# Kernel tuning notes

Measured on AMD Instinct MI355X. Metric: run time of the kernel, lower is better.

Reference implementation:

```python
import jax, jax.numpy as jnp
import numpy as np

HEADS = 8

def setup_inputs() -> dict:
    key = jax.random.key(0)
    k1, k2, k3 = jax.random.split(key, 3)
    B, C, L = 8, 512, 4096
    dim_head = 64
    hidden = HEADS * dim_head  # 512
    x = jax.random.normal(k1, (B, C, L), dtype=jnp.float32)
    # Conv1d(dim, hidden*3, 1, bias=False) -> weight [hidden*3, dim]
    w_qkv = jax.random.normal(k2, (hidden * 3, C), dtype=jnp.float32) * 0.02
    # Conv1d(hidden, dim, 1) -> weight [dim, hidden], bias [dim]
    w_out = jax.random.normal(k3, (C, hidden), dtype=jnp.float32) * 0.02
    b_out = jnp.zeros((C,), dtype=jnp.float32)
    return {"x": x, "w_qkv": w_qkv, "w_out": w_out, "b_out": b_out}

def reference(x, w_qkv, w_out, b_out):
    B, C, L = x.shape
    # 1x1 Conv1d == channel matmul
    qkv = jnp.einsum('oc,bcl->bol', w_qkv, x)            # [B, 3*H*dh, L]
    qkv = qkv.reshape(B, 3, HEADS, -1, L)                # qkv outermost, then heads, then c
    q, k, v = qkv[:, 0], qkv[:, 1], qkv[:, 2]            # each [B, H, dh, L]
    k = jax.nn.softmax(k, axis=-1)                       # softmax over sequence
    context = jnp.einsum('bhdn,bhen->bhde', k, v)        # [B, H, dh, dh]
    out = jnp.einsum('bhde,bhdn->bhen', context, q)      # [B, H, dh, L]
    out = out.reshape(B, -1, L)                          # [B, H*dh, L]
    return jnp.einsum('oc,bcl->bol', w_out, out) + b_out[None, :, None]
```

## Files before the change

### kernel.cpp

```cpp
#include <hip/hip_runtime.h>
#include <hip/hip_bf16.h>


typedef __bf16 bf16x8 __attribute__((ext_vector_type(8)));
typedef __bf16 bf16x4 __attribute__((ext_vector_type(4)));
typedef float  f32x4  __attribute__((ext_vector_type(4)));

#define B_  8
#define L_  4096
#define C_  512

#define GLD_LDS16(g, l)                                             \
    __builtin_amdgcn_global_load_lds(                               \
        (const __attribute__((address_space(1))) void*)(g),         \
        (__attribute__((address_space(3))) void*)(l), 16, 0, 0)

#define FENCE asm volatile("" ::: "memory")
#define BAR   do { FENCE; __builtin_amdgcn_s_barrier(); FENCE; } while (0)
#define DRAIN_LGKM asm volatile("s_waitcnt lgkmcnt(0)" ::: "memory")
#define WAIT_VM(N) asm volatile("s_waitcnt vmcnt(" #N ")" ::: "memory")

__global__ __launch_bounds__(256) void prep_all(const float* __restrict__ x,
                                                __hip_bfloat16* __restrict__ xt,
                                                const float* __restrict__ wqkv_f,
                                                __hip_bfloat16* __restrict__ wkv_b,
                                                __hip_bfloat16* __restrict__ wqT) {
    __shared__ float tile[64 * 133];
    int blk = blockIdx.x;
    int t = threadIdx.x;
    if (blk < 2048) {
        int b = blk >> 8, rem = blk & 255;
        int l0 = (rem & 31) * 128, c0 = (rem >> 5) * 64;
        const float* xp = x + ((size_t)b * C_ + c0) * L_ + l0;
#pragma unroll
        for (int p = 0; p < 8; p++) {
            int i = p * 8 + (t >> 5);
            int j = (t & 31) * 4;
            float4 vv = *(const float4*)(xp + (size_t)i * L_ + j);
            *(float4*)&tile[i * 133 + j] = vv;
        }
        __syncthreads();
        unsigned short* xo = (unsigned short*)xt + ((size_t)b * L_ + l0) * C_ + c0;
        int cg8 = (t & 7) * 8;
#pragma unroll
        for (int qq = 0; qq < 4; qq++) {
            int l = qq * 32 + (t >> 3);
            bf16x8 ov;
#pragma unroll
            for (int k = 0; k < 8; k++) ov[k] = (__bf16)tile[(cg8 + k) * 133 + l];
            *(bf16x8*)(xo + (size_t)l * C_ + cg8) = ov;
        }
    } else if (blk < 4096) {
        int i = (blk - 2048) * 256 + t;
        wkv_b[i] = __float2bfloat16(wqkv_f[512 * 512 + i]);
    } else {
        int tb = blk - 4096;
        int r0 = (tb >> 4) * 32, c0 = (tb & 15) * 32;
        int tx = t & 31, ty = t >> 5;
        for (int r = 0; r < 32; r += 8)
            tile[(ty + r) * 33 + tx] = wqkv_f[(size_t)(r0 + ty + r) * 512 + c0 + tx];
        __syncthreads();
        for (int r = 0; r < 32; r += 8)
            wqT[(size_t)(c0 + ty + r) * 512 + r0 + tx] = __float2bfloat16(tile[tx * 33 + ty + r]);
    }
}

template <int MODE>
__global__ __launch_bounds__(256, 2) void gemm_p(
    const __hip_bfloat16* __restrict__ A, const __hip_bfloat16* __restrict__ Bt,
    size_t strideA, size_t strideB, int M, int N, int K,
    __hip_bfloat16* __restrict__ kb, __hip_bfloat16* __restrict__ vb,
    __hip_bfloat16* __restrict__ obf,
    float* __restrict__ outb, const float* __restrict__ bias) {
    __shared__ alignas(16) unsigned short sA[2][128 * 64];
    __shared__ alignas(16) unsigned short sB[2][128 * 64];

    int b = blockIdx.z;
    int m0 = blockIdx.y * 128, n0 = blockIdx.x * 128;
    const __hip_bfloat16* Ab = A + strideA * (size_t)b;
    const __hip_bfloat16* Bb = Bt + strideB * (size_t)b;

    int t = threadIdx.x;
    int lane = t & 63, wv = t >> 6;
    int l16 = lane & 15, q4 = lane >> 4;
    int wr = (wv >> 1) * 64, wc = (wv & 1) * 64;

    int srow = lane >> 3;
    int swz  = ((lane & 7) ^ srow) * 8;

    const __hip_bfloat16* gA[4];
    const __hip_bfloat16* gB[4];
    unsigned ldoff[4];
#pragma unroll
    for (int c = 0; c < 4; c++) {
        int r = c * 32 + wv * 8;
        gA[c] = Ab + (size_t)(m0 + r + srow) * K + swz;
        gB[c] = Bb + (size_t)(n0 + r + srow) * K + swz;
        ldoff[c] = (unsigned)r * 64;
    }

    int gsel0 = (q4 ^ (l16 & 7)) * 8;
    int gsel1 = gsel0 ^ 32;
    unsigned rA = (unsigned)(wr + l16) * 64;
    unsigned rB = (unsigned)(wc + l16) * 64;
    int NKT = K >> 6;

    f32x4 acc[4][4] = {};
    bf16x8 aF[4][2], bF[4][2];

#pragma unroll
    for (int c = 0; c < 4; c++) GLD_LDS16(gA[c], &sA[0][ldoff[c]]);
#pragma unroll
    for (int c = 0; c < 4; c++) GLD_LDS16(gB[c], &sB[0][ldoff[c]]);
    if (NKT > 1) {
#pragma unroll
        for (int c = 0; c < 4; c++) GLD_LDS16(gA[c] + 64, &sA[1][ldoff[c]]);
        WAIT_VM(4);
    } else {
        WAIT_VM(0);
    }
    BAR;

#pragma unroll 1
    for (int kt = 0; kt < NKT; ++kt) {
        int cur = kt & 1, nbuf = cur ^ 1;
        const unsigned short* As_b = sA[cur];
        const unsigned short* Bs_b = sB[cur];
        bool st1 = (kt + 1) < NKT;
        bool st2 = (kt + 2) < NKT;

#pragma unroll
        for (int i = 0; i < 4; i++) {
            aF[i][0] = *(const bf16x8*)&As_b[rA + i * 1024 + gsel0];
            aF[i][1] = *(const bf16x8*)&As_b[rA + i * 1024 + gsel1];
        }
#pragma unroll
        for (int j = 0; j < 2; j++) {
            bF[j][0] = *(const bf16x8*)&Bs_b[rB + j * 1024 + gsel0];
            bF[j][1] = *(const bf16x8*)&Bs_b[rB + j * 1024 + gsel1];
        }
        if (st1) {
            int ko = (kt + 1) << 6;
#pragma unroll
            for (int c = 0; c < 4; c++) GLD_LDS16(gB[c] + ko, &sB[nbuf][ldoff[c]]);
        }
        BAR;
        __builtin_amdgcn_s_setprio(1);
#pragma unroll
        for (int ks = 0; ks < 2; ks++)
#pragma unroll
            for (int i = 0; i < 4; i++)
#pragma unroll
                for (int j = 0; j < 2; j++)
                    acc[i][j] = __builtin_amdgcn_mfma_f32_16x16x32_bf16(aF[i][ks], bF[j][ks], acc[i][j], 0, 0, 0);
        __builtin_amdgcn_s_setprio(0);
        DRAIN_LGKM;
        BAR;

#pragma unroll
        for (int j = 2; j < 4; j++) {
            bF[j][0] = *(const bf16x8*)&Bs_b[rB + j * 1024 + gsel0];
            bF[j][1] = *(const bf16x8*)&Bs_b[rB + j * 1024 + gsel1];
        }
        if (st2) {
            int ko = (kt + 2) << 6;
#pragma unroll
            for (int c = 0; c < 4; c++) GLD_LDS16(gA[c] + ko, &sA[cur][ldoff[c]]);
        }
        BAR;
        __builtin_amdgcn_s_setprio(1);
#pragma unroll
        for (int ks = 0; ks < 2; ks++)
#pragma unroll
            for (int i = 0; i < 4; i++)
#pragma unroll
                for (int j = 0; j < 2; j++)
                    acc[i][2 + j] = __builtin_amdgcn_mfma_f32_16x16x32_bf16(aF[i][ks], bF[2 + j][ks], acc[i][2 + j], 0, 0, 0);
        __builtin_amdgcn_s_setprio(0);
        DRAIN_LGKM;
        if (st2) { WAIT_VM(4); } else { WAIT_VM(0); }
        BAR;
    }

#pragma unroll
    for (int i = 0; i < 4; i++)
#pragma unroll
        for (int j = 0; j < 4; j++)
#pragma unroll
            for (int r = 0; r < 4; r++) {
                int row = m0 + wr + i * 16 + q4 * 4 + r;
                int col = n0 + wc + j * 16 + l16;
                float val = acc[i][j][r];
                if (MODE == 1) {
                    bool isk = (m0 < 512);
                    __hip_bfloat16* dst = isk ? kb : vb;
                    if (isk) val = __expf(val);
                    dst[((size_t)b * 512 + (row & 511)) * (size_t)N + col] = __float2bfloat16(val);
                } else if (MODE == 3) {
                    obf[((size_t)b * 512 + row) * (size_t)N + col] = __float2bfloat16(val);
                } else {
                    outb[((size_t)b * M + row) * (size_t)N + col] = val + bias[row];
                }
            }
}

__global__ __launch_bounds__(256) void ctx_kernel(const __hip_bfloat16* __restrict__ ek,
                                                  const __hip_bfloat16* __restrict__ v,
                                                  float* __restrict__ ctxp,
                                                  float* __restrict__ Sp) {
    int bx = blockIdx.x;
    int kc = bx >> 1, dh = bx & 1;
    int h = blockIdx.y, b = blockIdx.z;
    int t = threadIdx.x, lane = t & 63, wv = t >> 6;
    int l16 = lane & 15, q4 = lane >> 4;
    const __hip_bfloat16* ka = ek + ((size_t)b * 512 + h * 64 + dh * 32) * L_;
    const __hip_bfloat16* va = v + ((size_t)b * 512 + h * 64) * L_;

    f32x4 acc[2][4] = {};
    float ps[2] = {0.f, 0.f};
    int nbase = kc * 512 + wv * 128;
#pragma unroll
    for (int s = 0; s < 4; s++) {
        int n = nbase + s * 32 + q4 * 8;
        bf16x8 af[2], bfr[4];
#pragma unroll
        for (int i = 0; i < 2; i++) {
            af[i] = *(const bf16x8*)(ka + (size_t)(i * 16 + l16) * L_ + n);
#pragma unroll
            for (int e = 0; e < 8; e++) ps[i] += (float)af[i][e];
        }
#pragma unroll
        for (int j = 0; j < 4; j++)
            bfr[j] = *(const bf16x8*)(va + (size_t)(j * 16 + l16) * L_ + n);
#pragma unroll
        for (int i = 0; i < 2; i++)
#pragma unroll
            for (int j = 0; j < 4; j++)
                acc[i][j] = __builtin_amdgcn_mfma_f32_16x16x32_bf16(af[i], bfr[j], acc[i][j], 0, 0, 0);
    }

    __shared__ float sred[4][32];
#pragma unroll
    for (int i = 0; i < 2; i++) {
        ps[i] += __shfl_xor(ps[i], 16, 64);
        ps[i] += __shfl_xor(ps[i], 32, 64);
    }
    if (q4 == 0) {
#pragma unroll
        for (int i = 0; i < 2; i++) sred[wv][i * 16 + l16] = ps[i];
    }

    __shared__ float cbuf[2048];
    __syncthreads();
    for (int w = 0; w < 4; w++) {
        if (wv == w) {
#pragma unroll
            for (int i = 0; i < 2; i++)
#pragma unroll
                for (int j = 0; j < 4; j++)
#pragma unroll
                    for (int r = 0; r < 4; r++) {
                        int mm = i * 16 + q4 * 4 + r, nn = j * 16 + l16;
                        float pv = acc[i][j][r];
                        if (w == 0) cbuf[mm * 64 + nn] = pv;
                        else        cbuf[mm * 64 + nn] += pv;
                    }
        }
        __syncthreads();
    }
    float* cg = ctxp + ((size_t)kc * 64 + b * 8 + h) * 4096 + dh * 2048;
    for (int i = t; i < 2048; i += 256) cg[i] = cbuf[i];
    if (t < 32)
        Sp[((size_t)kc * 64 + b * 8 + h) * 64 + dh * 32 + t] =
            sred[0][t] + sred[1][t] + sred[2][t] + sred[3][t];
}

__global__ __launch_bounds__(256) void w2_kernel(const float* __restrict__ wout,
                                                 const float* __restrict__ ctxp,
                                                 const float* __restrict__ Sp,
                                                 __hip_bfloat16* __restrict__ w2) {
    int ob = blockIdx.x, h = blockIdx.y, b = blockIdx.z;
    __shared__ float cT[64 * 65];
    __shared__ float wT[64 * 65];
    __shared__ float Sinv[64];
    int t = threadIdx.x;
    const size_t SL = (size_t)64 * 4096;
    const float* cg = ctxp + ((size_t)b * 8 + h) * 4096;
    if (t < 64) {
        const float* sg = Sp + ((size_t)b * 8 + h) * 64;
        float S = 0.f;
#pragma unroll
        for (int s = 0; s < 8; s++) S += sg[(size_t)s * 64 * 64 + t];
        Sinv[t] = 1.0f / S;
    }
    __syncthreads();
#pragma unroll
    for (int it = 0; it < 4; ++it) {
        int i0 = (t + it * 256) * 4;
        int d = i0 >> 6, e0 = i0 & 63;
        float4 s4 = {0.f, 0.f, 0.f, 0.f};
#pragma unroll
        for (int sl = 0; sl < 8; sl++) {
            float4 vv = *(const float4*)&cg[(size_t)sl * SL + i0];
            s4.x += vv.x; s4.y += vv.y; s4.z += vv.z; s4.w += vv.w;
        }
        float si = Sinv[d];
        float4 wv4 = *(const float4*)&wout[(size_t)(ob * 64 + d) * 512 + h * 64 + e0];
        cT[(e0 + 0) * 65 + d] = s4.x * si;
        cT[(e0 + 1) * 65 + d] = s4.y * si;
        cT[(e0 + 2) * 65 + d] = s4.z * si;
        cT[(e0 + 3) * 65 + d] = s4.w * si;
        wT[(e0 + 0) * 65 + d] = wv4.x;
        wT[(e0 + 1) * 65 + d] = wv4.y;
        wT[(e0 + 2) * 65 + d] = wv4.z;
        wT[(e0 + 3) * 65 + d] = wv4.w;
    }
    __syncthreads();
    int ol = t >> 2;
    int db = (t & 3) * 16;
    unsigned short* w2p = (unsigned short*)w2 + ((size_t)b * 512 + ob * 64 + ol) * 512 + h * 64;
    for (int g = 0; g < 4; g++) {
        int d0 = db + g * 4;
        float s0 = 0.f, s1 = 0.f, s2 = 0.f, s3 = 0.f;
#pragma unroll
        for (int e = 0; e < 64; e++) {
            float w = wT[e * 65 + ol];
            s0 += w * cT[e * 65 + d0];
            s1 += w * cT[e * 65 + d0 + 1];
            s2 += w * cT[e * 65 + d0 + 2];
            s3 += w * cT[e * 65 + d0 + 3];
        }
        bf16x4 ov;
        ov[0] = (__bf16)s0; ov[1] = (__bf16)s1; ov[2] = (__bf16)s2; ov[3] = (__bf16)s3;
        *(bf16x4*)(w2p + d0) = ov;
    }
}

extern "C" void kernel_launch(void* const* d_in, const int* in_sizes, int n_in,
                              void* d_out, int out_size, void* d_ws, size_t ws_size,
                              hipStream_t stream) {
    const float* x     = (const float*)d_in[0];
    const float* w_qkv = (const float*)d_in[1];
    const float* w_out = (const float*)d_in[2];
    const float* b_out = (const float*)d_in[3];
    float* out = (float*)d_out;
    char* ws = (char*)d_ws;

    const size_t QKV = (size_t)B_ * 512 * L_;
    size_t off_xt   = 0;
    size_t off_wkv  = off_xt + (size_t)B_ * L_ * C_ * 2;
    size_t off_wqT  = off_wkv + (size_t)1024 * 512 * 2;
    size_t off_k    = off_wqT + (size_t)512 * 512 * 2;
    size_t off_v    = off_k + QKV * 2;
    size_t off_ctxp = off_v + QKV * 2;
    size_t off_Sp   = off_ctxp + (size_t)8 * 64 * 4096 * 4;
    size_t off_w2   = off_k;
    size_t off_w3   = off_k + (size_t)B_ * 512 * 512 * 2;

    __hip_bfloat16* xt   = (__hip_bfloat16*)(ws + off_xt);
    __hip_bfloat16* wkvb = (__hip_bfloat16*)(ws + off_wkv);
    __hip_bfloat16* wqT  = (__hip_bfloat16*)(ws + off_wqT);
    __hip_bfloat16* kb   = (__hip_bfloat16*)(ws + off_k);
    __hip_bfloat16* vb   = (__hip_bfloat16*)(ws + off_v);
    float*          ctxp = (float*)(ws + off_ctxp);
    float*          Sp   = (float*)(ws + off_Sp);
    __hip_bfloat16* w2   = (__hip_bfloat16*)(ws + off_w2);
    __hip_bfloat16* W3   = (__hip_bfloat16*)(ws + off_w3);

    prep_all<<<4352, 256, 0, stream>>>(x, xt, w_qkv, wkvb, wqT);

    gemm_p<1><<<dim3(L_ / 128, 1024 / 128, B_), 256, 0, stream>>>(
        wkvb, xt, 0, (size_t)L_ * C_, 1024, L_, 512, kb, vb, nullptr, nullptr, nullptr);

    ctx_kernel<<<dim3(16, 8, B_), 256, 0, stream>>>(kb, vb, ctxp, Sp);

    w2_kernel<<<dim3(8, 8, B_), 256, 0, stream>>>(w_out, ctxp, Sp, w2);

    gemm_p<3><<<dim3(512 / 128, 512 / 128, B_), 256, 0, stream>>>(
        w2, wqT, (size_t)512 * 512, 0, 512, 512, 512, nullptr, nullptr, W3, nullptr, nullptr);

    gemm_p<2><<<dim3(L_ / 128, 512 / 128, B_), 256, 0, stream>>>(
        W3, xt, (size_t)512 * 512, (size_t)L_ * C_, 512, L_, 512, nullptr, nullptr, nullptr, out, b_out);
}
```

Before: 243.6 us.

## Halve GEMM K-tile to 32 and raise occupancy to four blocks per CU

The GEMM K-tile shrinks from 64 to 32, halving LDS per block (32 KB instead of 64 KB), and launch bounds rise from 2 to 4 blocks per CU. The pipeline is restructured into one LDS read phase and one MFMA phase per iteration, with A and B for tile kt+2 both prefetched into the buffer just consumed. This aims to hide latency through more resident waves instead of intra-block interleaving. The cost is twice as many barrier-separated iterations with less MFMA work each, plus tighter register limits that could cause spills.

```diff
diff --git a/kernel.cpp b/kernel.cpp
--- a/kernel.cpp
+++ b/kernel.cpp
@@ -66,14 +66,14 @@
 }
 
 template <int MODE>
-__global__ __launch_bounds__(256, 2) void gemm_p(
+__global__ __launch_bounds__(256, 4) void gemm_p(
     const __hip_bfloat16* __restrict__ A, const __hip_bfloat16* __restrict__ Bt,
     size_t strideA, size_t strideB, int M, int N, int K,
     __hip_bfloat16* __restrict__ kb, __hip_bfloat16* __restrict__ vb,
     __hip_bfloat16* __restrict__ obf,
     float* __restrict__ outb, const float* __restrict__ bias) {
-    __shared__ alignas(16) unsigned short sA[2][128 * 64];
-    __shared__ alignas(16) unsigned short sB[2][128 * 64];
+    __shared__ alignas(16) unsigned short sA[2][128 * 32];
+    __shared__ alignas(16) unsigned short sB[2][128 * 32];
 
     int b = blockIdx.z;
     int m0 = blockIdx.y * 128, n0 = blockIdx.x * 128;
@@ -85,99 +85,70 @@
     int l16 = lane & 15, q4 = lane >> 4;
     int wr = (wv >> 1) * 64, wc = (wv & 1) * 64;
 
-    int srow = lane >> 3;
-    int swz  = ((lane & 7) ^ srow) * 8;
-
-    const __hip_bfloat16* gA[4];
-    const __hip_bfloat16* gB[4];
-    unsigned ldoff[4];
-#pragma unroll
-    for (int c = 0; c < 4; c++) {
-        int r = c * 32 + wv * 8;
-        gA[c] = Ab + (size_t)(m0 + r + srow) * K + swz;
-        gB[c] = Bb + (size_t)(n0 + r + srow) * K + swz;
-        ldoff[c] = (unsigned)r * 64;
-    }
-
-    int gsel0 = (q4 ^ (l16 & 7)) * 8;
-    int gsel1 = gsel0 ^ 32;
-    unsigned rA = (unsigned)(wr + l16) * 64;
-    unsigned rB = (unsigned)(wc + l16) * 64;
-    int NKT = K >> 6;
+    int srow = lane >> 2;
+    int swz  = ((lane & 3) ^ (srow & 3)) * 8;
+
+    const __hip_bfloat16* gA[2];
+    const __hip_bfloat16* gB[2];
+    unsigned ldoff[2];
+#pragma unroll
+    for (int c = 0; c < 2; c++) {
+        int lr = c * 64 + wv * 16 + srow;
+        gA[c] = Ab + (size_t)(m0 + lr) * K + swz;
+        gB[c] = Bb + (size_t)(n0 + lr) * K + swz;
+        ldoff[c] = (unsigned)(c * 64 + wv * 16) * 32;
+    }
+
+    int gsel = (q4 ^ (l16 & 3)) * 8;
+    unsigned rA = (unsigned)(wr + l16) * 32;
+    unsigned rB = (unsigned)(wc + l16) * 32;
+    const int NKT = K >> 5;
 
     f32x4 acc[4][4] = {};
-    bf16x8 aF[4][2], bF[4][2];
-
-#pragma unroll
-    for (int c = 0; c < 4; c++) GLD_LDS16(gA[c], &sA[0][ldoff[c]]);
-#pragma unroll
-    for (int c = 0; c < 4; c++) GLD_LDS16(gB[c], &sB[0][ldoff[c]]);
-    if (NKT > 1) {
-#pragma unroll
-        for (int c = 0; c < 4; c++) GLD_LDS16(gA[c] + 64, &sA[1][ldoff[c]]);
-        WAIT_VM(4);
-    } else {
-        WAIT_VM(0);
-    }
+    bf16x8 aF[4], bF[4];
+
+#pragma unroll
+    for (int c = 0; c < 2; c++) {
+        GLD_LDS16(gA[c], &sA[0][ldoff[c]]);
+        GLD_LDS16(gB[c], &sB[0][ldoff[c]]);
+    }
+#pragma unroll
+    for (int c = 0; c < 2; c++) {
+        GLD_LDS16(gA[c] + 32, &sA[1][ldoff[c]]);
+        GLD_LDS16(gB[c] + 32, &sB[1][ldoff[c]]);
+    }
+    WAIT_VM(4);
     BAR;
 
 #pragma unroll 1
     for (int kt = 0; kt < NKT; ++kt) {
-        int cur = kt & 1, nbuf = cur ^ 1;
+        int cur = kt & 1;
         const unsigned short* As_b = sA[cur];
         const unsigned short* Bs_b = sB[cur];
-        bool st1 = (kt + 1) < NKT;
         bool st2 = (kt + 2) < NKT;
 
 #pragma unroll
-        for (int i = 0; i < 4; i++) {
-            aF[i][0] = *(const bf16x8*)&As_b[rA + i * 1024 + gsel0];
-            aF[i][1] = *(const bf16x8*)&As_b[rA + i * 1024 + gsel1];
-        }
-#pragma unroll
-        for (int j = 0; j < 2; j++) {
-            bF[j][0] = *(const bf16x8*)&Bs_b[rB + j * 1024 + gsel0];
-            bF[j][1] = *(const bf16x8*)&Bs_b[rB + j * 1024 + gsel1];
-        }
-        if (st1) {
-            int ko = (kt + 1) << 6;
-#pragma unroll
-            for (int c = 0; c < 4; c++) GLD_LDS16(gB[c] + ko, &sB[nbuf][ldoff[c]]);
-        }
-        BAR;
-        __builtin_amdgcn_s_setprio(1);
-#pragma unroll
-        for (int ks = 0; ks < 2; ks++)
-#pragma unroll
-            for (int i = 0; i < 4; i++)
-#pragma unroll
-                for (int j = 0; j < 2; j++)
-                    acc[i][j] = __builtin_amdgcn_mfma_f32_16x16x32_bf16(aF[i][ks], bF[j][ks], acc[i][j], 0, 0, 0);
-        __builtin_amdgcn_s_setprio(0);
+        for (int i = 0; i < 4; i++) aF[i] = *(const bf16x8*)&As_b[rA + i * 512 + gsel];
+#pragma unroll
+        for (int j = 0; j < 4; j++) bF[j] = *(const bf16x8*)&Bs_b[rB + j * 512 + gsel];
         DRAIN_LGKM;
         BAR;
 
-#pragma unroll
-        for (int j = 2; j < 4; j++) {
-            bF[j][0] = *(const bf16x8*)&Bs_b[rB + j * 1024 + gsel0];
-            bF[j][1] = *(const bf16x8*)&Bs_b[rB + j * 1024 + gsel1];
-        }
         if (st2) {
-            int ko = (kt + 2) << 6;
-#pragma unroll
-            for (int c = 0; c < 4; c++) GLD_LDS16(gA[c] + ko, &sA[cur][ldoff[c]]);
-        }
-        BAR;
+            int ko = (kt + 2) << 5;
+#pragma unroll
+            for (int c = 0; c < 2; c++) {
+                GLD_LDS16(gA[c] + ko, &sA[cur][ldoff[c]]);
+                GLD_LDS16(gB[c] + ko, &sB[cur][ldoff[c]]);
+            }
+        }
         __builtin_amdgcn_s_setprio(1);
 #pragma unroll
-        for (int ks = 0; ks < 2; ks++)
-#pragma unroll
-            for (int i = 0; i < 4; i++)
-#pragma unroll
-                for (int j = 0; j < 2; j++)
-                    acc[i][2 + j] = __builtin_amdgcn_mfma_f32_16x16x32_bf16(aF[i][ks], bF[2 + j][ks], acc[i][2 + j], 0, 0, 0);
+        for (int i = 0; i < 4; i++)
+#pragma unroll
+            for (int j = 0; j < 4; j++)
+                acc[i][j] = __builtin_amdgcn_mfma_f32_16x16x32_bf16(aF[i], bF[j], acc[i][j], 0, 0, 0);
         __builtin_amdgcn_s_setprio(0);
-        DRAIN_LGKM;
         if (st2) { WAIT_VM(4); } else { WAIT_VM(0); }
         BAR;
     }
```

Result: no change. 248.2 us (+1.9%).
